# Optimization experiments

Hardware: AMD Instinct MI355X
Metric: run time of the kernel (lower is better)

## Reference

```python
import jax, jax.numpy as jnp
import numpy as np

B, L, D, M = 8, 2048, 512, 256
D2, H = 2 * D, 4 * D  # attention d_model, FFN hidden
EPS = 1e-6


def setup_inputs() -> dict:
    key = jax.random.key(0)
    ks = jax.random.split(key, 16)
    s2 = 1.0 / np.sqrt(D2)
    sD = 1.0 / np.sqrt(D)
    sH = 1.0 / np.sqrt(H)
    f32 = jnp.float32
    return {
        "zr": jax.random.normal(ks[0], (B, L, D), f32),
        "zi": jax.random.normal(ks[1], (B, L, D), f32),
        "Wq": jax.random.normal(ks[2], (D2, D2), f32) * s2,
        "Wk": jax.random.normal(ks[3], (D2, D2), f32) * s2,
        "Wv": jax.random.normal(ks[4], (D2, D2), f32) * s2,
        "Wo": jax.random.normal(ks[5], (D2, D2), f32) * s2,
        "Wf": jax.random.normal(ks[6], (M, D2), f32),  # trainable random features (std normal, FAVOR+)
        "b_attn": jnp.zeros((D,), f32),
        "W1r": jax.random.normal(ks[7], (D, H), f32) * sD,
        "W1i": jax.random.normal(ks[8], (D, H), f32) * sD,
        "b1r": jnp.zeros((H,), f32),
        "b1i": jnp.zeros((H,), f32),
        "W2r": jax.random.normal(ks[9], (H, D), f32) * sH,
        "W2i": jax.random.normal(ks[10], (H, D), f32) * sH,
        "b2r": jnp.zeros((D,), f32),
        "b2i": jnp.zeros((D,), f32),
        "b_ffn": jnp.zeros((D,), f32),
    }


def modrelu(xr, xi, b):
    # ModReLU: relu(|z| + b) * z / |z|, per-channel bias b
    mag = jnp.sqrt(xr * xr + xi * xi + EPS)
    s = jax.nn.relu(mag + b) / mag
    return xr * s, xi * s


def _block(zr, zi, Wq, Wk, Wv, Wo, Wf, b_attn,
           W1r, W1i, b1r, b1i, W2r, W2i, b2r, b2i, b_ffn):
    # --- kernelized linear attention on real/imag concat [B,L,2D] ---
    x = jnp.concatenate([zr, zi], axis=-1)
    scl = D2 ** -0.25
    q = (x @ Wq) * scl
    k = (x @ Wk) * scl
    v = x @ Wv
    # FAVOR+ positive features: phi(u) = exp(Wf u - |u|^2/2) / sqrt(m)
    pq = q @ Wf.T - 0.5 * jnp.sum(q * q, axis=-1, keepdims=True)  # [B,L,M]
    pk = k @ Wf.T - 0.5 * jnp.sum(k * k, axis=-1, keepdims=True)
    phi_q = jnp.exp(pq - jax.lax.stop_gradient(jnp.max(pq, axis=-1, keepdims=True))) / np.sqrt(M)
    phi_k = jnp.exp(pk - jax.lax.stop_gradient(jnp.max(pk))) / np.sqrt(M)
    kv = jnp.einsum('blm,bld->bmd', phi_k, v)              # [B,M,2D]
    den = jnp.einsum('blm,bm->bl', phi_q, phi_k.sum(axis=1))  # [B,L]
    y = jnp.einsum('blm,bmd->bld', phi_q, kv) / (den[..., None] + EPS)
    y = y @ Wo
    yr, yi = y[..., :D], y[..., D:]
    # Add & Norm (ModReLU)
    zr, zi = modrelu(zr + yr, zi + yi, b_attn)
    # --- complex FFN: complex Linear -> CReLU -> complex Linear ---
    hr = zr @ W1r - zi @ W1i + b1r
    hi = zr @ W1i + zi @ W1r + b1i
    hr = jax.nn.relu(hr)
    hi = jax.nn.relu(hi)
    fr = hr @ W2r - hi @ W2i + b2r
    fi = hr @ W2i + hi @ W2r + b2i
    # Add & Norm (ModReLU)
    zr, zi = modrelu(zr + fr, zi + fi, b_ffn)
    return jnp.stack([zr, zi], axis=-1)  # [B,L,D,2]


def reference(zr, zi, Wq, Wk, Wv, Wo, Wf, b_attn,
              W1r, W1i, b1r, b1i, W2r, W2i, b2r, b2i, b_ffn):
    return _block(zr, zi, Wq, Wk, Wv, Wo, Wf, b_attn,
                  W1r, W1i, b1r, b1i, W2r, W2i, b2r, b2i, b_ffn)
```

## Files before the change

kernel.cpp:

```cpp
#include <hip/hip_runtime.h>
#include <math.h>

#define B_ 8
#define L_ 2048
#define D_ 512
#define M_ 256
#define D2_ 1024
#define H_ 2048
#define N_ 16384
#define EPS_ 1e-6f

typedef __attribute__((ext_vector_type(8))) short bf16x8;
typedef __attribute__((ext_vector_type(4))) float f32x4;
typedef unsigned short ushort_t;
typedef unsigned int uint_t;

#define WAITCNT_VM8 0x0F78
#define WAITCNT_VM6 0x0F76
#define WAITCNT_VM4 0x0F74
#define WAITCNT_VM0 0x0F70

__device__ __forceinline__ ushort_t f2bf(float f) {
    uint_t u = __float_as_uint(f);
    u += 0x7FFFu + ((u >> 16) & 1u);
    return (ushort_t)(u >> 16);
}
__device__ __forceinline__ float bf2f(ushort_t u) {
    return __uint_as_float(((uint_t)u) << 16);
}
__device__ __forceinline__ void gload_lds16(const void* g, void* l) {
    __builtin_amdgcn_global_load_lds(
        (const __attribute__((address_space(1))) void*)g,
        (__attribute__((address_space(3))) void*)l, 16, 0, 0);
}

__global__ __launch_bounds__(256)
void gemm_mfma(const ushort_t* __restrict__ A, const ushort_t* __restrict__ Bm,
               void* __restrict__ Cp, int K, int lda, int ldb, int ldc,
               long long sA, long long sB, long long sC,
               int epi, float alpha, const float* __restrict__ aux,
               int auxStride, const float* __restrict__ bias, int obf)
{
    __shared__ ushort_t As[4][128 * 32];
    __shared__ ushort_t Bs[4][128 * 32];

    const int bz = blockIdx.z;
    A  += (long long)bz * sA;
    Bm += (long long)bz * sB;
    const int row0 = blockIdx.y * 128;
    const int col0 = blockIdx.x * 128;

    const int tid  = threadIdx.x;
    const int lane = tid & 63;
    const int wave = tid >> 6;
    const int wr = wave >> 1, wc = wave & 1;

    const int srow = tid >> 2;
    const int skol = (((tid & 3) ^ ((tid >> 3) & 3)) * 8);

    f32x4 acc[4][4];
    #pragma unroll
    for (int i = 0; i < 4; ++i)
        #pragma unroll
        for (int j = 0; j < 4; ++j)
            acc[i][j] = (f32x4){0.f, 0.f, 0.f, 0.f};

    const int fr = lane & 15;
    const int fq = lane >> 4;
    const int koff = ((fq ^ ((fr >> 1) & 3))) * 8;

    const int nT = K >> 5;

    auto issue = [&](int t) {
        const int buf = t & 3;
        const int k0 = t << 5;
        gload_lds16(A + (long long)(row0 + srow) * lda + k0 + skol,
                    &As[buf][(wave * 16) * 32]);
        gload_lds16(A + (long long)(row0 + 64 + srow) * lda + k0 + skol,
                    &As[buf][(64 + wave * 16) * 32]);
        gload_lds16(Bm + (long long)(col0 + srow) * ldb + k0 + skol,
                    &Bs[buf][(wave * 16) * 32]);
        gload_lds16(Bm + (long long)(col0 + 64 + srow) * ldb + k0 + skol,
                    &Bs[buf][(64 + wave * 16) * 32]);
    };

    issue(0);
    if (nT > 1) issue(1);
    for (int t = 0; t < nT; ++t) {
        if (t + 2 < nT) {
            issue(t + 2);
            __builtin_amdgcn_s_waitcnt(WAITCNT_VM8);
        } else if (t + 1 < nT) {
            __builtin_amdgcn_s_waitcnt(WAITCNT_VM4);
        } else {
            __builtin_amdgcn_s_waitcnt(WAITCNT_VM0);
        }
        __builtin_amdgcn_s_barrier();

        const int cur = t & 3;
        bf16x8 a[4], b[4];
        #pragma unroll
        for (int i = 0; i < 4; ++i)
            a[i] = *(const bf16x8*)&As[cur][(wr * 64 + i * 16 + fr) * 32 + koff];
        #pragma unroll
        for (int j = 0; j < 4; ++j)
            b[j] = *(const bf16x8*)&Bs[cur][(wc * 64 + j * 16 + fr) * 32 + koff];
        #pragma unroll
        for (int i = 0; i < 4; ++i)
            #pragma unroll
            for (int j = 0; j < 4; ++j)
                acc[i][j] = __builtin_amdgcn_mfma_f32_16x16x32_bf16(
                    a[i], b[j], acc[i][j], 0, 0, 0);
    }

    const int gr0 = row0 + wr * 64;
    const int gc0 = col0 + wc * 64;
    #pragma unroll
    for (int i = 0; i < 4; ++i) {
        #pragma unroll
        for (int r = 0; r < 4; ++r) {
            const int row = gr0 + i * 16 + fq * 4 + r;
            float raux = 0.f;
            if (epi == 1 || epi == 2) raux = aux[(long long)bz * auxStride + row];
            #pragma unroll
            for (int j = 0; j < 4; ++j) {
                const int col = gc0 + j * 16 + fr;
                float v = acc[i][j][r];
                if (epi == 0)      v *= alpha;
                else if (epi == 1) v -= 0.5f * raux;
                else if (epi == 2) v = v / (raux + EPS_);
                else if (epi == 5) v -= 0.5f * aux[(long long)bz * auxStride + col];
                else if (epi == 3) { v += bias[col]; v = v > 0.f ? v : 0.f; }
                else if (epi == 4) v += bias[col];
                const long long off = (long long)bz * sC + (long long)row * ldc + col;
                if (obf) ((ushort_t*)Cp)[off] = f2bf(v);
                else     ((float*)Cp)[off] = v;
            }
        }
    }
}

__global__ __launch_bounds__(512, 2)
void gemm256(const ushort_t* __restrict__ A, const ushort_t* __restrict__ Bm,
             void* __restrict__ Cp, int K, int lda, int ldb, int ldc,
             long long sA, long long sB, long long sC,
             int epi, float alpha, const float* __restrict__ aux,
             int auxStride, const float* __restrict__ bias, int obf,
             int ksplit)
{
    __shared__ ushort_t As[2][256 * 64];
    __shared__ ushort_t Bs[2][256 * 64];

    const int gx = gridDim.x, gy = gridDim.y, gz = gridDim.z;
    {
    }
    int fid = blockIdx.x + gx * (blockIdx.y + gy * blockIdx.z);
    const int nwg = gx * gy * gz;
    const int qch = nwg >> 3, rch = nwg & 7;
    const int xcd = fid & 7, idx = fid >> 3;
    int nid = (xcd < rch ? xcd * (qch + 1) : rch * (qch + 1) + (xcd - rch) * qch)
              + idx;
    const int bx = nid % gx; nid /= gx;
    const int by = nid % gy;
    const int bzf = nid / gy;

    const int bz = bzf / ksplit;
    const int kz = bzf - bz * ksplit;
    const int Kh = K / ksplit;

    A  += (long long)bz * sA + (long long)kz * Kh;
    Bm += (long long)bz * sB + (long long)kz * Kh;
    const int row0 = by * 256;
    const int col0 = bx * 256;

    const int tid  = threadIdx.x;
    const int lane = tid & 63;
    const int wave = tid >> 6;
    const int wr   = wave >> 2;
    const int wcn  = wave & 3;

    const int rloc  = tid >> 3;
    const int csrc8 = (((tid & 7) ^ (rloc & 7)) << 3);

    const int fr = lane & 15;
    const int fq = lane >> 4;
    const int sw = fr & 7;
    const int c0off = ((fq ^ sw) << 3);
    const int c1off = (((4 | fq) ^ sw) << 3);

    const int nT = Kh >> 6;

    f32x4 acc[8][4];
    #pragma unroll
    for (int i = 0; i < 8; ++i)
        #pragma unroll
        for (int j = 0; j < 4; ++j)
            acc[i][j] = (f32x4){0.f, 0.f, 0.f, 0.f};

    bf16x8 a[4][2];
    bf16x8 b[4][2];

    auto stage = [&](int bufS, int tS, int half) {
        const int k0 = tS << 6;
        const int rh = (half >= 2) ? 1 : 0;
        const bool isA = (half == 0 || half == 3);
        const ushort_t* g = isA
            ? A  + (long long)(row0 + rh * 128 + rloc) * lda + k0 + csrc8
            : Bm + (long long)(col0 + rh * 128 + rloc) * ldb + k0 + csrc8;
        const long long gstep = 64LL * (isA ? lda : ldb);
        ushort_t* l = (isA ? &As[bufS][0] : &Bs[bufS][0])
                      + (rh * 128 + wave * 8) * 64;
        gload_lds16(g, l);
        gload_lds16(g + gstep, l + 64 * 64);
    };

    auto ldsA = [&](int buf, int mh, int i, int koff) -> bf16x8 {
        return *(const bf16x8*)
            &As[buf][(wr * 128 + mh * 64 + i * 16 + fr) * 64 + koff];
    };
    auto ldsB = [&](int buf, int j, int koff) -> bf16x8 {
        return *(const bf16x8*)
            &Bs[buf][(wcn * 64 + j * 16 + fr) * 64 + koff];
    };

    stage(0, 0, 0); stage(0, 0, 1); stage(0, 0, 2); stage(0, 0, 3);
    stage(1, 1, 0); stage(1, 1, 1); stage(1, 1, 2);
    __builtin_amdgcn_s_waitcnt(WAITCNT_VM6);
    __builtin_amdgcn_s_barrier();

    auto tile_body = [&](int t, int buf) {
        #pragma unroll
        for (int i = 0; i < 4; ++i) {
            a[i][0] = ldsA(buf, 0, i, c0off);
            a[i][1] = ldsA(buf, 0, i, c1off);
        }
        #pragma unroll
        for (int j = 0; j < 2; ++j) {
            b[j][0] = ldsB(buf, j, c0off);
            b[j][1] = ldsB(buf, j, c1off);
        }
        if (t + 1 < nT) stage(buf ^ 1, t + 1, 3);
        __builtin_amdgcn_s_barrier();
        asm volatile("s_waitcnt lgkmcnt(0)" ::: "memory");
        __builtin_amdgcn_s_setprio(1);
        #pragma unroll
        for (int i = 0; i < 4; ++i)
            #pragma unroll
            for (int j = 0; j < 2; ++j) {
                acc[i][j] = __builtin_amdgcn_mfma_f32_16x16x32_bf16(
                    a[i][0], b[j][0], acc[i][j], 0, 0, 0);
                acc[i][j] = __builtin_amdgcn_mfma_f32_16x16x32_bf16(
                    a[i][1], b[j][1], acc[i][j], 0, 0, 0);
            }
        __builtin_amdgcn_s_setprio(0);
        __builtin_amdgcn_s_barrier();

        #pragma unroll
        for (int j = 2; j < 4; ++j) {
            b[j][0] = ldsB(buf, j, c0off);
            b[j][1] = ldsB(buf, j, c1off);
        }
        __builtin_amdgcn_s_barrier();
        asm volatile("s_waitcnt lgkmcnt(0)" ::: "memory");
        __builtin_amdgcn_s_setprio(1);
        #pragma unroll
        for (int i = 0; i < 4; ++i)
            #pragma unroll
            for (int j = 2; j < 4; ++j) {
                acc[i][j] = __builtin_amdgcn_mfma_f32_16x16x32_bf16(
                    a[i][0], b[j][0], acc[i][j], 0, 0, 0);
                acc[i][j] = __builtin_amdgcn_mfma_f32_16x16x32_bf16(
                    a[i][1], b[j][1], acc[i][j], 0, 0, 0);
            }
        __builtin_amdgcn_s_setprio(0);
        __builtin_amdgcn_s_barrier();

        #pragma unroll
        for (int i = 0; i < 4; ++i) {
            a[i][0] = ldsA(buf, 1, i, c0off);
            a[i][1] = ldsA(buf, 1, i, c1off);
        }
        if (t + 2 < nT) stage(buf, t + 2, 1);
        __builtin_amdgcn_s_barrier();
        asm volatile("s_waitcnt lgkmcnt(0)" ::: "memory");
        __builtin_amdgcn_s_setprio(1);
        #pragma unroll
        for (int i = 0; i < 4; ++i)
            #pragma unroll
            for (int j = 2; j < 4; ++j) {
                acc[4 + i][j] = __builtin_amdgcn_mfma_f32_16x16x32_bf16(
                    a[i][0], b[j][0], acc[4 + i][j], 0, 0, 0);
                acc[4 + i][j] = __builtin_amdgcn_mfma_f32_16x16x32_bf16(
                    a[i][1], b[j][1], acc[4 + i][j], 0, 0, 0);
            }
        __builtin_amdgcn_s_setprio(0);
        __builtin_amdgcn_s_barrier();

        if (t + 2 < nT) { stage(buf, t + 2, 2); stage(buf, t + 2, 0); }
        __builtin_amdgcn_s_barrier();
        asm volatile("s_waitcnt lgkmcnt(0)" ::: "memory");
        __builtin_amdgcn_s_setprio(1);
        #pragma unroll
        for (int i = 0; i < 4; ++i)
            #pragma unroll
            for (int j = 0; j < 2; ++j) {
                acc[4 + i][j] = __builtin_amdgcn_mfma_f32_16x16x32_bf16(
                    a[i][0], b[j][0], acc[4 + i][j], 0, 0, 0);
                acc[4 + i][j] = __builtin_amdgcn_mfma_f32_16x16x32_bf16(
                    a[i][1], b[j][1], acc[4 + i][j], 0, 0, 0);
            }
        __builtin_amdgcn_s_setprio(0);
        if (t + 2 < nT)      __builtin_amdgcn_s_waitcnt(WAITCNT_VM6);
        else if (t + 1 < nT) __builtin_amdgcn_s_waitcnt(WAITCNT_VM0);
        __builtin_amdgcn_s_barrier();
    };

    for (int t = 0; t < nT; t += 2) {
        tile_body(t, 0);
        tile_body(t + 1, 1);
    }

    const int gr0 = row0 + wr * 128;
    const int gc0 = col0 + wcn * 64;
    #pragma unroll
    for (int i = 0; i < 8; ++i) {
        #pragma unroll
        for (int r = 0; r < 4; ++r) {
            const int row = gr0 + i * 16 + fq * 4 + r;
            float raux = 0.f;
            if (epi == 1 || epi == 2) raux = aux[(long long)bz * auxStride + row];
            #pragma unroll
            for (int j = 0; j < 4; ++j) {
                const int col = gc0 + j * 16 + fr;
                float v = acc[i][j][r];
                const long long off = (long long)bz * sC + (long long)row * ldc + col;
                if (ksplit > 1) {
                    atomicAdd((float*)Cp + off, v * alpha);
                    continue;
                }
                if (epi == 0)      v *= alpha;
                else if (epi == 1) v -= 0.5f * raux;
                else if (epi == 2) v = v / (raux + EPS_);
                else if (epi == 5) v -= 0.5f * aux[(long long)bz * auxStride + col];
                else if (epi == 3) { v += bias[col]; v = v > 0.f ? v : 0.f; }
                else if (epi == 4) v += bias[col];
                if (obf) ((ushort_t*)Cp)[off] = f2bf(v);
                else     ((float*)Cp)[off] = v;
            }
        }
    }
}

__global__ __launch_bounds__(256)
void seed_c(const float* __restrict__ bias, float* __restrict__ C)
{
    const long long t = (long long)blockIdx.x * 256 + threadIdx.x;
    C[t] = bias ? bias[(int)(t & (D2_ - 1))] : 0.f;
}


__global__ __launch_bounds__(256)
void transpose_cvt_sq(const float* __restrict__ W, ushort_t* __restrict__ out)
{
    __shared__ float S[32][33];
    const int tx = threadIdx.x & 31, ty = threadIdx.x >> 5;
    const int n0 = blockIdx.x * 32, k0 = blockIdx.y * 32;
    #pragma unroll
    for (int r = 0; r < 4; ++r)
        S[ty + 8 * r][tx] = W[(long long)(k0 + ty + 8 * r) * 1024 + n0 + tx];
    __syncthreads();
    #pragma unroll
    for (int r = 0; r < 4; ++r)
        out[(long long)(n0 + ty + 8 * r) * 1024 + k0 + tx] = f2bf(S[tx][ty + 8 * r]);
}

__global__ __launch_bounds__(256)
void build_wc1T(const float* __restrict__ W1r, const float* __restrict__ W1i,
                ushort_t* __restrict__ out)
{
    __shared__ float S[32][33];
    const int tx = threadIdx.x & 31, ty = threadIdx.x >> 5;
    const int i0 = blockIdx.x * 32, j0 = blockIdx.y * 32;
    #pragma unroll
    for (int r = 0; r < 4; ++r) {
        const int i = i0 + ty + 8 * r, j = j0 + tx;
        float v;
        if (j < H_) v = (i < D_) ? W1r[(long long)i * H_ + j]
                                 : -W1i[(long long)(i - D_) * H_ + j];
        else {
            const int jj = j - H_;
            v = (i < D_) ? W1i[(long long)i * H_ + jj]
                         : W1r[(long long)(i - D_) * H_ + jj];
        }
        S[tx][ty + 8 * r] = v;
    }
    __syncthreads();
    #pragma unroll
    for (int r = 0; r < 4; ++r)
        out[(long long)(j0 + ty + 8 * r) * 1024 + i0 + tx] = f2bf(S[ty + 8 * r][tx]);
}

__global__ __launch_bounds__(256)
void build_wc2T(const float* __restrict__ W2r, const float* __restrict__ W2i,
                ushort_t* __restrict__ out)
{
    __shared__ float S[32][33];
    const int tx = threadIdx.x & 31, ty = threadIdx.x >> 5;
    const int i0 = blockIdx.x * 32, j0 = blockIdx.y * 32;
    #pragma unroll
    for (int r = 0; r < 4; ++r) {
        const int i = i0 + ty + 8 * r, j = j0 + tx;
        float v;
        if (i < H_) v = (j < D_) ? W2r[(long long)i * D_ + j]
                                 : W2i[(long long)i * D_ + (j - D_)];
        else {
            const int ii = i - H_;
            v = (j < D_) ? -W2i[(long long)ii * D_ + j]
                         : W2r[(long long)ii * D_ + (j - D_)];
        }
        S[tx][ty + 8 * r] = v;
    }
    __syncthreads();
    #pragma unroll
    for (int r = 0; r < 4; ++r)
        out[(long long)(j0 + ty + 8 * r) * 4096 + i0 + tx] = f2bf(S[ty + 8 * r][tx]);
}

__global__ __launch_bounds__(256)
void build_bias(const float* __restrict__ b1r, const float* __restrict__ b1i,
                const float* __restrict__ b2r, const float* __restrict__ b2i,
                float* __restrict__ bc1, float* __restrict__ bc2)
{
    const int t = blockIdx.x * 256 + threadIdx.x;
    bc1[t] = (t < H_) ? b1r[t] : b1i[t - H_];
    if (t < D2_) bc2[t] = (t < D_) ? b2r[t] : b2i[t - D_];
}

__global__ __launch_bounds__(256)
void cvt_Wf(const float* __restrict__ Wf, ushort_t* __restrict__ out)
{
    const int t = blockIdx.x * 256 + threadIdx.x;
    out[t] = f2bf(Wf[t]);
}

__global__ __launch_bounds__(256)
void cvt_x(const float* __restrict__ zr, const float* __restrict__ zi,
           ushort_t* __restrict__ x)
{
    long long t = (long long)blockIdx.x * 256 + threadIdx.x;
    long long n = t >> 8;
    int j4 = (int)(t & 255) << 2;
    float4 v;
    if (j4 < D_) v = *(const float4*)(zr + n * D_ + j4);
    else         v = *(const float4*)(zi + n * D_ + (j4 - D_));
    uint2 o;
    o.x = (uint_t)f2bf(v.x) | ((uint_t)f2bf(v.y) << 16);
    o.y = (uint_t)f2bf(v.z) | ((uint_t)f2bf(v.w) << 16);
    *(uint2*)(x + n * D2_ + j4) = o;
}

__global__ __launch_bounds__(256)
void rowsumsq_bf(const ushort_t* __restrict__ A, float* __restrict__ out)
{
    const int wid = threadIdx.x >> 6, lane = threadIdx.x & 63;
    const long long row = (long long)blockIdx.x * 4 + wid;
    const ushort_t* a = A + row * D2_;
    float s = 0.f;
    #pragma unroll
    for (int h = 0; h < 2; ++h) {
        uint4 u = *(const uint4*)(a + h * 512 + lane * 8);
        const uint_t w[4] = {u.x, u.y, u.z, u.w};
        #pragma unroll
        for (int p = 0; p < 4; ++p) {
            float lo = bf2f((ushort_t)(w[p] & 0xffff));
            float hi = bf2f((ushort_t)(w[p] >> 16));
            s += lo * lo + hi * hi;
        }
    }
    #pragma unroll
    for (int off = 32; off; off >>= 1) s += __shfl_down(s, off, 64);
    if (lane == 0) out[row] = s;
}

__global__ __launch_bounds__(256)
void phi_rowmax_exp(const float* __restrict__ P, ushort_t* __restrict__ out)
{
    const long long row = blockIdx.x;
    const int t = threadIdx.x;
    const float v = P[row * M_ + t];
    float m = v;
    #pragma unroll
    for (int off = 32; off; off >>= 1) m = fmaxf(m, __shfl_down(m, off, 64));
    __shared__ float sm[4];
    const int wid = t >> 6, lane = t & 63;
    if (lane == 0) sm[wid] = m;
    __syncthreads();
    const float mm = fmaxf(fmaxf(sm[0], sm[1]), fmaxf(sm[2], sm[3]));
    out[row * M_ + t] = f2bf(expf(v - mm) * 0.0625f);
}

__global__ __launch_bounds__(256)
void gmax1(const float* __restrict__ P, float* __restrict__ part, int n)
{
    float m = -3.4e38f;
    for (long long i = (long long)blockIdx.x * 256 + threadIdx.x; i < n;
         i += (long long)gridDim.x * 256)
        m = fmaxf(m, P[i]);
    #pragma unroll
    for (int off = 32; off; off >>= 1) m = fmaxf(m, __shfl_down(m, off, 64));
    __shared__ float sm[4];
    const int wid = threadIdx.x >> 6, lane = threadIdx.x & 63;
    if (lane == 0) sm[wid] = m;
    __syncthreads();
    if (threadIdx.x == 0)
        part[blockIdx.x] = fmaxf(fmaxf(sm[0], sm[1]), fmaxf(sm[2], sm[3]));
}

__global__ __launch_bounds__(256)
void gmax2(float* __restrict__ red)
{
    float m = -3.4e38f;
    for (int i = threadIdx.x; i < 1024; i += 256) m = fmaxf(m, red[256 + i]);
    #pragma unroll
    for (int off = 32; off; off >>= 1) m = fmaxf(m, __shfl_down(m, off, 64));
    __shared__ float sm[4];
    const int wid = threadIdx.x >> 6, lane = threadIdx.x & 63;
    if (lane == 0) sm[wid] = m;
    __syncthreads();
    if (threadIdx.x == 0) red[0] = fmaxf(fmaxf(sm[0], sm[1]), fmaxf(sm[2], sm[3]));
}

__global__ __launch_bounds__(256)
void phikT_exp(const float* __restrict__ P, const float* __restrict__ red,
               ushort_t* __restrict__ out)
{
    const long long i = (long long)blockIdx.x * 256 + threadIdx.x;
    out[i] = f2bf(expf(P[i] - red[0]) * 0.0625f);
}

__global__ __launch_bounds__(256)
void ksum_k(const ushort_t* __restrict__ phikT, float* __restrict__ ks)
{
    const int b = blockIdx.x >> 8, m = blockIdx.x & 255;
    const ushort_t* p = phikT + (long long)m * N_ + b * L_;
    uint4 u = *(const uint4*)(p + threadIdx.x * 8);
    const uint_t w[4] = {u.x, u.y, u.z, u.w};
    float s = 0.f;
    #pragma unroll
    for (int q = 0; q < 4; ++q)
        s += bf2f((ushort_t)(w[q] & 0xffff)) + bf2f((ushort_t)(w[q] >> 16));
    #pragma unroll
    for (int off = 32; off; off >>= 1) s += __shfl_down(s, off, 64);
    __shared__ float sm[4];
    const int wid = threadIdx.x >> 6, lane = threadIdx.x & 63;
    if (lane == 0) sm[wid] = s;
    __syncthreads();
    if (threadIdx.x == 0)
        ks[blockIdx.x] = sm[0] + sm[1] + sm[2] + sm[3];
}

__global__ __launch_bounds__(256)
void den_k(const ushort_t* __restrict__ phiq, const float* __restrict__ ks,
           float* __restrict__ den)
{
    const int wid = threadIdx.x >> 6, lane = threadIdx.x & 63;
    const long long n = (long long)blockIdx.x * 4 + wid;
    const int b = (int)(n >> 11);
    uint2 u = *(const uint2*)(phiq + n * M_ + lane * 4);
    float4 kk = *(const float4*)(ks + b * M_ + lane * 4);
    float s = bf2f((ushort_t)(u.x & 0xffff)) * kk.x
            + bf2f((ushort_t)(u.x >> 16)) * kk.y
            + bf2f((ushort_t)(u.y & 0xffff)) * kk.z
            + bf2f((ushort_t)(u.y >> 16)) * kk.w;
    #pragma unroll
    for (int off = 32; off; off >>= 1) s += __shfl_down(s, off, 64);
    if (lane == 0) den[n] = s;
}

__global__ __launch_bounds__(256)
void modrelu_attn(const float* __restrict__ zr, const float* __restrict__ zi,
                  const float* __restrict__ yo, const float* __restrict__ b_attn,
                  ushort_t* __restrict__ zst)
{
    const long long t = (long long)blockIdx.x * 256 + threadIdx.x;
    const long long n = t >> 9; const int d = (int)(t & 511);
    const float ar = zr[t] + yo[n * D2_ + d];
    const float ai = zi[t] + yo[n * D2_ + D_ + d];
    const float mag = sqrtf(ar * ar + ai * ai + EPS_);
    const float s = fmaxf(mag + b_attn[d], 0.f) / mag;
    zst[n * D2_ + d]      = f2bf(ar * s);
    zst[n * D2_ + D_ + d] = f2bf(ai * s);
}

__global__ __launch_bounds__(256)
void modrelu_out(const ushort_t* __restrict__ zst, const float* __restrict__ f,
                 const float* __restrict__ b_ffn, float* __restrict__ out)
{
    const long long t = (long long)blockIdx.x * 256 + threadIdx.x;
    const long long n = t >> 9; const int d = (int)(t & 511);
    const float ar = bf2f(zst[n * D2_ + d])      + f[n * D2_ + d];
    const float ai = bf2f(zst[n * D2_ + D_ + d]) + f[n * D2_ + D_ + d];
    const float mag = sqrtf(ar * ar + ai * ai + EPS_);
    const float s = fmaxf(mag + b_ffn[d], 0.f) / mag;
    out[t * 2]     = ar * s;
    out[t * 2 + 1] = ai * s;
}

extern "C" void kernel_launch(void* const* d_in, const int* in_sizes, int n_in,
                              void* d_out, int out_size, void* d_ws, size_t ws_size,
                              hipStream_t stream)
{
    const float* zr    = (const float*)d_in[0];
    const float* zi    = (const float*)d_in[1];
    const float* Wq    = (const float*)d_in[2];
    const float* Wk    = (const float*)d_in[3];
    const float* Wv    = (const float*)d_in[4];
    const float* Wo    = (const float*)d_in[5];
    const float* Wf    = (const float*)d_in[6];
    const float* b_attn= (const float*)d_in[7];
    const float* W1r   = (const float*)d_in[8];
    const float* W1i   = (const float*)d_in[9];
    const float* b1r   = (const float*)d_in[10];
    const float* b1i   = (const float*)d_in[11];
    const float* W2r   = (const float*)d_in[12];
    const float* W2i   = (const float*)d_in[13];
    const float* b2r   = (const float*)d_in[14];
    const float* b2i   = (const float*)d_in[15];
    const float* b_ffn = (const float*)d_in[16];

    char* w = (char*)d_ws;
    ushort_t* Xbf = (ushort_t*)(w + 0LL);
    ushort_t* A1  = (ushort_t*)(w + 33554432LL);
    float*    P   = (float*)   (w + 67108864LL);
    ushort_t* WqT = (ushort_t*)(w + 83886080LL);
    ushort_t* WkT = (ushort_t*)(w + 85983232LL);
    ushort_t* WvT = (ushort_t*)(w + 88080384LL);
    ushort_t* Wfb = (ushort_t*)(w + 90177536LL);
    ushort_t* F1  = (ushort_t*)(w + 100663296LL);
    ushort_t* F2  = (ushort_t*)(w + 109051904LL);
    ushort_t* WoT = (ushort_t*)(w + 117440512LL);
    ushort_t* KVT = (ushort_t*)(w + 119537664LL);
    float* ssqq = (float*)(w + 123731968LL);
    float* ssqk = (float*)(w + 123797504LL);
    float* den  = (float*)(w + 123863040LL);
    float* ksum = (float*)(w + 123928576LL);
    float* red  = (float*)(w + 123936768LL);

    const bool big = ws_size >= 152000000ULL;
    const int  RCH = big ? 8192 : 4096;
    ushort_t* Hb = (ushort_t*)(w + 33554432LL);
    float* Fb  = big ? (float*)(w + 117440512LL) : (float*)(w + 67108864LL);
    float* bc1 = big ? (float*)(w + 150994944LL) : (float*)(w + 123944960LL);
    float* bc2 = big ? (float*)(w + 151011328LL) : (float*)(w + 123961344LL);

    const float scl = 0.1767766952966369f;
    dim3 blk(256);

    auto GM = [&](const ushort_t* A, const ushort_t* Bm, void* C,
                  int rows, int cols, int K, int lda, int ldb, int ldc,
                  long long sA, long long sB, long long sC, int nb,
                  int epi, float alpha, const float* aux, int auxStride,
                  const float* bias, int obf) {
        const long long wg256 = (long long)(cols >> 8) * (rows >> 8) * nb;
        if ((rows & 255) == 0 && (cols & 255) == 0 && (K & 127) == 0 &&
            wg256 >= 128) {
            dim3 grid(cols / 256, rows / 256, nb);
            gemm256<<<grid, dim3(512), 0, stream>>>(A, Bm, C, K, lda, ldb, ldc,
                                                    sA, sB, sC, epi, alpha, aux,
                                                    auxStride, bias, obf, 1);
        } else {
            dim3 grid(cols / 128, rows / 128, nb);
            gemm_mfma<<<grid, blk, 0, stream>>>(A, Bm, C, K, lda, ldb, ldc,
                                                sA, sB, sC, epi, alpha, aux,
                                                auxStride, bias, obf);
        }
    };

    transpose_cvt_sq<<<dim3(32, 32), blk, 0, stream>>>(Wq, WqT);
    transpose_cvt_sq<<<dim3(32, 32), blk, 0, stream>>>(Wk, WkT);
    transpose_cvt_sq<<<dim3(32, 32), blk, 0, stream>>>(Wv, WvT);
    transpose_cvt_sq<<<dim3(32, 32), blk, 0, stream>>>(Wo, WoT);
    cvt_Wf<<<1024, blk, 0, stream>>>(Wf, Wfb);
    build_bias<<<16, blk, 0, stream>>>(b1r, b1i, b2r, b2i, bc1, bc2);
    cvt_x<<<N_ * (D2_ / 4) / 256, blk, 0, stream>>>(zr, zi, Xbf);

    GM(Xbf, WqT, A1, N_, D2_, D2_, D2_, D2_, D2_, 0, 0, 0, 1, 0, scl, nullptr, 0, nullptr, 1);
    rowsumsq_bf<<<N_ / 4, blk, 0, stream>>>(A1, ssqq);
    GM(A1, Wfb, P, N_, M_, D2_, D2_, D2_, M_, 0, 0, 0, 1, 1, 1.f, ssqq, 0, nullptr, 0);
    phi_rowmax_exp<<<N_, blk, 0, stream>>>(P, F1);

    GM(Xbf, WkT, A1, N_, D2_, D2_, D2_, D2_, D2_, 0, 0, 0, 1, 0, scl, nullptr, 0, nullptr, 1);
    rowsumsq_bf<<<N_ / 4, blk, 0, stream>>>(A1, ssqk);
    GM(Wfb, A1, P, M_, N_, D2_, D2_, D2_, N_, 0, 0, 0, 1, 5, 1.f, ssqk, 0, nullptr, 0);
    gmax1<<<1024, blk, 0, stream>>>(P, red + 256, M_ * N_);
    gmax2<<<1, blk, 0, stream>>>(red);
    phikT_exp<<<M_ * N_ / 256, blk, 0, stream>>>(P, red, F2);

    GM(WvT, Xbf, A1, D2_, N_, D2_, D2_, D2_, N_, 0, 0, 0, 1, 0, 1.f, nullptr, 0, nullptr, 1);

    ksum_k<<<B_ * M_, blk, 0, stream>>>(F2, ksum);
    GM(A1, F2, KVT, D2_, M_, L_, N_, N_, M_, L_, L_, (long long)D2_ * M_, B_,
       0, 1.f, nullptr, 0, nullptr, 1);

    den_k<<<N_ / 4, blk, 0, stream>>>(F1, ksum, den);
    GM(F1, KVT, A1, L_, D2_, M_, M_, M_, D2_, (long long)L_ * M_,
       (long long)D2_ * M_, (long long)L_ * D2_, B_, 2, 1.f, den, L_, nullptr, 1);

    for (int c = 0; c < 2; ++c) {
        const long long ro = (long long)c * 8192;
        GM(A1 + ro * D2_, WoT, P, 8192, D2_, D2_, D2_, D2_, D2_, 0, 0, 0, 1,
           0, 1.f, nullptr, 0, nullptr, 0);
        modrelu_attn<<<8192 * D_ / 256, blk, 0, stream>>>(
            zr + ro * D_, zi + ro * D_, P, b_attn, Xbf + ro * D2_);
    }

    build_wc1T<<<dim3(32, 128), blk, 0, stream>>>(W1r, W1i, F1);
    build_wc2T<<<dim3(128, 32), blk, 0, stream>>>(W2r, W2i, F2);

    for (int c = 0; c < N_ / RCH; ++c) {
        const long long ro = (long long)c * RCH;
        GM(Xbf + ro * D2_, F1, Hb, RCH, 2 * H_, D2_, D2_, D2_, 2 * H_,
           0, 0, 0, 1, 3, 1.f, nullptr, 0, bc1, 1);
        if (RCH == 8192) {
            seed_c<<<RCH * D2_ / 256, blk, 0, stream>>>(bc2, Fb);
            dim3 grid2(D2_ / 256, RCH / 256, 2);
            gemm256<<<grid2, dim3(512), 0, stream>>>(
                Hb, F2, Fb, 2 * H_, 2 * H_, 2 * H_, D2_,
                0, 0, 0, 4, 1.f, nullptr, 0, bc2, 0, 2);
        } else {
            GM(Hb, F2, Fb, RCH, D2_, 2 * H_, 2 * H_, 2 * H_, D2_,
               0, 0, 0, 1, 4, 1.f, nullptr, 0, bc2, 0);
        }
        modrelu_out<<<RCH * D_ / 256, blk, 0, stream>>>(
            Xbf + ro * D2_, Fb, b_ffn, (float*)d_out + ro * D2_);
    }

    (void)in_sizes; (void)n_in; (void)out_size;
}
```

Measured before the change: 1.121 ms.

## Restructure GEMM mainloop to four-stage K=32 LDS ring with simpler phases

Replaces the double-buffered K=64 tile pipeline in gemm256 with a four-buffer ring of K=32 tiles. Each iteration now runs two MFMA phases instead of four, with A and B prefetched two tiles ahead and a new LDS swizzle suited to 32-element rows. This aims to deepen prefetch and cut barriers per K unit while keeping the same LDS footprint. In exchange there are more loop iterations and more barriers per unit of K, and the wait counts and swizzle must be exactly right.

```diff
diff --git a/kernel.cpp b/kernel.cpp
--- a/kernel.cpp
+++ b/kernel.cpp
@@ -148,12 +148,10 @@
              int auxStride, const float* __restrict__ bias, int obf,
              int ksplit)
 {
-    __shared__ ushort_t As[2][256 * 64];
-    __shared__ ushort_t Bs[2][256 * 64];
+    __shared__ ushort_t As[4][256 * 32];
+    __shared__ ushort_t Bs[4][256 * 32];
 
     const int gx = gridDim.x, gy = gridDim.y, gz = gridDim.z;
-    {
-    }
     int fid = blockIdx.x + gx * (blockIdx.y + gy * blockIdx.z);
     const int nwg = gx * gy * gz;
     const int qch = nwg >> 3, rch = nwg & 7;
@@ -179,16 +177,14 @@
     const int wr   = wave >> 2;
     const int wcn  = wave & 3;
 
-    const int rloc  = tid >> 3;
-    const int csrc8 = (((tid & 7) ^ (rloc & 7)) << 3);
+    const int srow = tid >> 2;
+    const int skol = (((tid & 3) ^ ((tid >> 3) & 3)) << 3);
 
     const int fr = lane & 15;
     const int fq = lane >> 4;
-    const int sw = fr & 7;
-    const int c0off = ((fq ^ sw) << 3);
-    const int c1off = (((4 | fq) ^ sw) << 3);
-
-    const int nT = Kh >> 6;
+    const int koff = ((fq ^ ((fr >> 1) & 3)) << 3);
+
+    const int nT = Kh >> 5;
 
     f32x4 acc[8][4];
     #pragma unroll
@@ -197,127 +193,69 @@
         for (int j = 0; j < 4; ++j)
             acc[i][j] = (f32x4){0.f, 0.f, 0.f, 0.f};
 
-    bf16x8 a[4][2];
-    bf16x8 b[4][2];
-
-    auto stage = [&](int bufS, int tS, int half) {
-        const int k0 = tS << 6;
-        const int rh = (half >= 2) ? 1 : 0;
-        const bool isA = (half == 0 || half == 3);
-        const ushort_t* g = isA
-            ? A  + (long long)(row0 + rh * 128 + rloc) * lda + k0 + csrc8
-            : Bm + (long long)(col0 + rh * 128 + rloc) * ldb + k0 + csrc8;
-        const long long gstep = 64LL * (isA ? lda : ldb);
-        ushort_t* l = (isA ? &As[bufS][0] : &Bs[bufS][0])
-                      + (rh * 128 + wave * 8) * 64;
-        gload_lds16(g, l);
-        gload_lds16(g + gstep, l + 64 * 64);
+    bf16x8 a[4], b[4];
+
+    const ushort_t* Ar0 = A  + (long long)(row0 + srow)       * lda + skol;
+    const ushort_t* Ar1 = A  + (long long)(row0 + 128 + srow) * lda + skol;
+    const ushort_t* Br0 = Bm + (long long)(col0 + srow)       * ldb + skol;
+    const ushort_t* Br1 = Bm + (long long)(col0 + 128 + srow) * ldb + skol;
+
+    auto stageA = [&](int t) {
+        const int buf = t & 3;
+        const int k0 = t << 5;
+        gload_lds16(Ar0 + k0, &As[buf][(wave * 16) * 32]);
+        gload_lds16(Ar1 + k0, &As[buf][(128 + wave * 16) * 32]);
     };
-
-    auto ldsA = [&](int buf, int mh, int i, int koff) -> bf16x8 {
-        return *(const bf16x8*)
-            &As[buf][(wr * 128 + mh * 64 + i * 16 + fr) * 64 + koff];
+    auto stageB = [&](int t) {
+        const int buf = t & 3;
+        const int k0 = t << 5;
+        gload_lds16(Br0 + k0, &Bs[buf][(wave * 16) * 32]);
+        gload_lds16(Br1 + k0, &Bs[buf][(128 + wave * 16) * 32]);
     };
-    auto ldsB = [&](int buf, int j, int koff) -> bf16x8 {
-        return *(const bf16x8*)
-            &Bs[buf][(wcn * 64 + j * 16 + fr) * 64 + koff];
-    };
-
-    stage(0, 0, 0); stage(0, 0, 1); stage(0, 0, 2); stage(0, 0, 3);
-    stage(1, 1, 0); stage(1, 1, 1); stage(1, 1, 2);
-    __builtin_amdgcn_s_waitcnt(WAITCNT_VM6);
+
+    stageA(0); stageB(0);
+    stageA(1); stageB(1);
+    __builtin_amdgcn_s_waitcnt(WAITCNT_VM4);
     __builtin_amdgcn_s_barrier();
 
-    auto tile_body = [&](int t, int buf) {
-        #pragma unroll
-        for (int i = 0; i < 4; ++i) {
-            a[i][0] = ldsA(buf, 0, i, c0off);
-            a[i][1] = ldsA(buf, 0, i, c1off);
-        }
-        #pragma unroll
-        for (int j = 0; j < 2; ++j) {
-            b[j][0] = ldsB(buf, j, c0off);
-            b[j][1] = ldsB(buf, j, c1off);
-        }
-        if (t + 1 < nT) stage(buf ^ 1, t + 1, 3);
+    for (int t = 0; t < nT; ++t) {
+        const int buf = t & 3;
+        #pragma unroll
+        for (int i = 0; i < 4; ++i)
+            a[i] = *(const bf16x8*)&As[buf][(wr * 128 + i * 16 + fr) * 32 + koff];
+        #pragma unroll
+        for (int j = 0; j < 4; ++j)
+            b[j] = *(const bf16x8*)&Bs[buf][(wcn * 64 + j * 16 + fr) * 32 + koff];
+        if (t + 2 < nT) stageA(t + 2);
         __builtin_amdgcn_s_barrier();
         asm volatile("s_waitcnt lgkmcnt(0)" ::: "memory");
         __builtin_amdgcn_s_setprio(1);
         #pragma unroll
         for (int i = 0; i < 4; ++i)
             #pragma unroll
-            for (int j = 0; j < 2; ++j) {
+            for (int j = 0; j < 4; ++j)
                 acc[i][j] = __builtin_amdgcn_mfma_f32_16x16x32_bf16(
-                    a[i][0], b[j][0], acc[i][j], 0, 0, 0);
-                acc[i][j] = __builtin_amdgcn_mfma_f32_16x16x32_bf16(
-                    a[i][1], b[j][1], acc[i][j], 0, 0, 0);
-            }
+                    a[i], b[j], acc[i][j], 0, 0, 0);
         __builtin_amdgcn_s_setprio(0);
         __builtin_amdgcn_s_barrier();
 
         #pragma unroll
-        for (int j = 2; j < 4; ++j) {
-            b[j][0] = ldsB(buf, j, c0off);
-            b[j][1] = ldsB(buf, j, c1off);
-        }
+        for (int i = 0; i < 4; ++i)
+            a[i] = *(const bf16x8*)&As[buf][(wr * 128 + 64 + i * 16 + fr) * 32 + koff];
+        if (t + 2 < nT) stageB(t + 2);
         __builtin_amdgcn_s_barrier();
         asm volatile("s_waitcnt lgkmcnt(0)" ::: "memory");
         __builtin_amdgcn_s_setprio(1);
         #pragma unroll
         for (int i = 0; i < 4; ++i)
             #pragma unroll
-            for (int j = 2; j < 4; ++j) {
-                acc[i][j] = __builtin_amdgcn_mfma_f32_16x16x32_bf16(
-                    a[i][0], b[j][0], acc[i][j], 0, 0, 0);
-                acc[i][j] = __builtin_amdgcn_mfma_f32_16x16x32_bf16(
-                    a[i][1], b[j][1], acc[i][j], 0, 0, 0);
-            }
+            for (int j = 0; j < 4; ++j)
+                acc[4 + i][j] = __builtin_amdgcn_mfma_f32_16x16x32_bf16(
+                    a[i], b[j], acc[4 + i][j], 0, 0, 0);
         __builtin_amdgcn_s_setprio(0);
-        __builtin_amdgcn_s_barrier();
-
-        #pragma unroll
-        for (int i = 0; i < 4; ++i) {
-            a[i][0] = ldsA(buf, 1, i, c0off);
-            a[i][1] = ldsA(buf, 1, i, c1off);
-        }
-        if (t + 2 < nT) stage(buf, t + 2, 1);
-        __builtin_amdgcn_s_barrier();
-        asm volatile("s_waitcnt lgkmcnt(0)" ::: "memory");
-        __builtin_amdgcn_s_setprio(1);
-        #pragma unroll
-        for (int i = 0; i < 4; ++i)
-            #pragma unroll
-            for (int j = 2; j < 4; ++j) {
-                acc[4 + i][j] = __builtin_amdgcn_mfma_f32_16x16x32_bf16(
-                    a[i][0], b[j][0], acc[4 + i][j], 0, 0, 0);
-                acc[4 + i][j] = __builtin_amdgcn_mfma_f32_16x16x32_bf16(
-                    a[i][1], b[j][1], acc[4 + i][j], 0, 0, 0);
-            }
-        __builtin_amdgcn_s_setprio(0);
-        __builtin_amdgcn_s_barrier();
-
-        if (t + 2 < nT) { stage(buf, t + 2, 2); stage(buf, t + 2, 0); }
-        __builtin_amdgcn_s_barrier();
-        asm volatile("s_waitcnt lgkmcnt(0)" ::: "memory");
-        __builtin_amdgcn_s_setprio(1);
-        #pragma unroll
-        for (int i = 0; i < 4; ++i)
-            #pragma unroll
-            for (int j = 0; j < 2; ++j) {
-                acc[4 + i][j] = __builtin_amdgcn_mfma_f32_16x16x32_bf16(
-                    a[i][0], b[j][0], acc[4 + i][j], 0, 0, 0);
-                acc[4 + i][j] = __builtin_amdgcn_mfma_f32_16x16x32_bf16(
-                    a[i][1], b[j][1], acc[4 + i][j], 0, 0, 0);
-            }
-        __builtin_amdgcn_s_setprio(0);
-        if (t + 2 < nT)      __builtin_amdgcn_s_waitcnt(WAITCNT_VM6);
+        if (t + 2 < nT)      __builtin_amdgcn_s_waitcnt(WAITCNT_VM4);
         else if (t + 1 < nT) __builtin_amdgcn_s_waitcnt(WAITCNT_VM0);
         __builtin_amdgcn_s_barrier();
-    };
-
-    for (int t = 0; t < nT; t += 2) {
-        tile_body(t, 0);
-        tile_body(t + 1, 1);
     }
 
     const int gr0 = row0 + wr * 128;
```

After: 1.466 ms. 30.8% more time.
